# Optimization experiments

Measured on AMD Instinct MI355X. Metric: run time of the kernel, lower is better.

## Reference

```python
import jax, jax.numpy as jnp
import numpy as np

CUTOFF = 5.0

def ssp(x):
    # shifted softplus: ln(0.5*e^x + 0.5)
    return jax.nn.softplus(x) - jnp.log(2.0).astype(x.dtype)

def cosine_cutoff(r):
    return 0.5 * (jnp.cos(jnp.pi * r / CUTOFF) + 1.0) * (r < CUTOFF).astype(r.dtype)

def setup_inputs() -> dict:
    key = jax.random.key(0)
    ks = jax.random.split(key, 16)
    B, A, N, Nd, F, Din, Dout, Th = 2, 512, 1024, 64, 64, 128, 128, 25
    inp = {}
    inp['x'] = jax.random.normal(ks[0], (B, A, Din), dtype=jnp.float32)
    inp['r_double'] = jax.random.uniform(ks[1], (B, A, Nd), dtype=jnp.float32)
    inp['r_ij'] = jax.random.uniform(ks[2], (B, A, N), dtype=jnp.float32)
    inp['r_ik'] = jax.random.uniform(ks[3], (B, A, N), dtype=jnp.float32)
    inp['r_jk'] = jax.random.uniform(ks[4], (B, A, N), dtype=jnp.float32)
    inp['neighbors'] = jax.random.randint(ks[5], (B, A, Nd), 0, A, dtype=jnp.int32)
    inp['neighbor_mask'] = jnp.ones((B, A, Nd), dtype=jnp.float32)
    inp['neighbors_j'] = jax.random.randint(ks[6], (B, A, N), 0, A, dtype=jnp.int32)
    inp['neighbors_k'] = jax.random.randint(ks[7], (B, A, N), 0, A, dtype=jnp.int32)
    inp['triple_masks'] = jnp.ones((B, A, N), dtype=jnp.float32)
    inp['d_ijk'] = jax.random.uniform(ks[8], (B, A, N, Th), dtype=jnp.float32)
    s = 0.1
    inp['W_in2f'] = s * jax.random.normal(ks[9], (Din, F), dtype=jnp.float32)
    inp['W_t1'] = s * jax.random.normal(ks[10], (Th, F), dtype=jnp.float32)
    inp['b_t1'] = jnp.zeros((F,), dtype=jnp.float32)
    inp['W_t2'] = s * jax.random.normal(ks[11], (F, F), dtype=jnp.float32)
    inp['b_t2'] = jnp.zeros((F,), dtype=jnp.float32)
    inp['W_f2out'] = s * jax.random.normal(ks[12], (F, Dout), dtype=jnp.float32)
    inp['b_f2out'] = jnp.zeros((Dout,), dtype=jnp.float32)
    return inp

def reference(x, r_double, r_ij, r_ik, r_jk, neighbors, neighbor_mask,
              neighbors_j, neighbors_k, triple_masks, d_ijk,
              W_in2f, W_t1, b_t1, W_t2, b_t2, W_f2out, b_f2out):
    # Triple filter: 2-layer MLP on angular basis, modulated by cutoffs
    h = ssp(jnp.einsum('bant,tf->banf', d_ijk, W_t1) + b_t1)
    W_triple = jnp.einsum('banf,fg->bang', h, W_t2) + b_t2
    W_triple = W_triple * cosine_cutoff(r_ij)[..., None] * cosine_cutoff(r_ik)[..., None]

    # in2f: (B, A, F)
    y = jnp.einsum('bad,df->baf', x, W_in2f)
    B, A, N = neighbors_j.shape
    F = y.shape[-1]
    # gather neighbor features along atom axis
    yj = jnp.take_along_axis(y, neighbors_j.reshape(B, A * N, 1), axis=1).reshape(B, A, N, F)
    yk = jnp.take_along_axis(y, neighbors_k.reshape(B, A * N, 1), axis=1).reshape(B, A, N, F)
    w_ij = r_ij[..., None]
    w_ik = r_ik[..., None]
    y = (w_ij * yj + w_ik * yk) / (w_ij + w_ik)
    # filter multiply + masked sum aggregation over triples axis
    y = y * W_triple
    y = jnp.sum(y * triple_masks[..., None], axis=2)
    # f2out with shifted-softplus activation
    out = ssp(jnp.einsum('baf,fo->bao', y, W_f2out) + b_f2out)
    return out
```

## Files before the change

kernel.cpp:

```cpp
#include <hip/hip_runtime.h>

#define BB 2
#define AA 512
#define NN 1024
#define FF 64
#define DIN 128
#define DOUT 128
#define TH 25
#define ASTRIDE 40
#define HSTRIDE 72
#define NSPLIT 4
#define BAN_TOTAL (BB * AA * NN)

typedef _Float16 half8 __attribute__((ext_vector_type(8)));
typedef _Float16 half2v __attribute__((ext_vector_type(2)));
typedef float floatx4 __attribute__((ext_vector_type(4)));

__device__ __forceinline__ float ssp_f(float x) {
    return __logf(0.5f * __expf(x) + 0.5f);
}

__device__ __forceinline__ float cutcos(float r) {
    float c = 0.5f * (__cosf(r * (3.14159265358979323846f / 5.0f)) + 1.0f);
    return (r < 5.0f) ? c : 0.0f;
}

#define OFF_Y       0
#define OFF_PARTIAL (OFF_Y + (size_t)BB * AA * FF * 2)
#define OFF_B1      (OFF_PARTIAL + (size_t)NSPLIT * BB * AA * FF * 4)
#define OFF_B2      (OFF_B1 + 4 * 64 * 8 * 2)
#define OFF_BC      (OFF_B2 + 8 * 64 * 8 * 2)
#define OFF_WTAB    (OFF_BC + 4 * 64 * 8)

__global__ void prep_kernel(const float* __restrict__ W_t1, const float* __restrict__ b_t1,
                            const float* __restrict__ W_t2, const float* __restrict__ b_t2,
                            _Float16* __restrict__ B1tab, _Float16* __restrict__ B2tab,
                            float2* __restrict__ bctab) {
    const int lane = threadIdx.x;
    const int quad = lane >> 4;
    const int l16 = lane & 15;
#pragma unroll
    for (int g = 0; g < 4; ++g) {
#pragma unroll
        for (int j = 0; j < 8; ++j) {
            int k = quad * 8 + j;
            B1tab[(g * 64 + lane) * 8 + j] =
                (k < TH) ? (_Float16)W_t1[k * FF + g * 16 + l16] : (_Float16)0.f;
        }
        bctab[g * 64 + lane] = make_float2(b_t1[g * 16 + l16], b_t2[g * 16 + l16]);
#pragma unroll
        for (int q = 0; q < 2; ++q)
#pragma unroll
            for (int j = 0; j < 8; ++j)
                B2tab[((g * 2 + q) * 64 + lane) * 8 + j] =
                    (_Float16)W_t2[(q * 32 + quad * 8 + j) * FF + g * 16 + l16];
    }
}

__global__ void wprep_kernel(const float* __restrict__ r_ij, const float* __restrict__ r_ik,
                             const float* __restrict__ tmask, half2v* __restrict__ wtab) {
    const int i = blockIdx.x * 256 + threadIdx.x;
    float rij = r_ij[i], rik = r_ik[i];
    float inv = cutcos(rij) * cutcos(rik) * tmask[i] / (rij + rik);
    half2v p;
    p[0] = (_Float16)(rij * inv);
    p[1] = (_Float16)(rik * inv);
    wtab[i] = p;
}

__global__ void in2f_kernel(const float* __restrict__ x,
                            const float* __restrict__ Wi,
                            _Float16* __restrict__ y) {
    __shared__ float xs[DIN];
    const int ba = blockIdx.x;
    const int t = threadIdx.x;
    xs[t] = x[ba * DIN + t];
    xs[t + 64] = x[ba * DIN + 64 + t];
    __syncthreads();
    float acc = 0.f;
#pragma unroll 8
    for (int d = 0; d < DIN; ++d) acc += xs[d] * Wi[d * FF + t];
    y[ba * FF + t] = (_Float16)acc;
}

__global__ __launch_bounds__(256) void triple_kernel(
    const int* __restrict__ nbrj, const int* __restrict__ nbrk,
    const float* __restrict__ d_ijk,
    const _Float16* __restrict__ B1tab, const _Float16* __restrict__ B2tab,
    const float2* __restrict__ bctab, const half2v* __restrict__ wtab,
    const _Float16* __restrict__ y_tab, float* __restrict__ partial) {

    __shared__ __align__(16) _Float16 a_tile[4][16 * ASTRIDE];
    __shared__ __align__(16) _Float16 h_tile[4][16 * HSTRIDE];
    __shared__ float red[4][FF];

    const int blk = blockIdx.x;
    const int ba = blk >> 2;
    const int split = blk & 3;
    const int b = ba >> 9;
    const int tid = threadIdx.x;
    const int w = tid >> 6;
    const int lane = tid & 63;
    const int quad = lane >> 4;
    const int l16 = lane & 15;
    const int rA = lane >> 3;
    const int fc = (lane & 7) * 8;

    const long ban = (long)ba * NN;
    const float* dbase = d_ijk + (long)ba * NN * TH;
    const _Float16* yb = y_tab + (long)b * (AA * FF);

    half8 B1[4];
    half8 B2[4][2];
    float b1v[4], b2v[4];
#pragma unroll
    for (int g = 0; g < 4; ++g) {
        B1[g] = *(const half8*)(B1tab + (g * 64 + lane) * 8);
        B2[g][0] = *(const half8*)(B2tab + ((g * 2 + 0) * 64 + lane) * 8);
        B2[g][1] = *(const half8*)(B2tab + ((g * 2 + 1) * 64 + lane) * 8);
        float2 bc = bctab[g * 64 + lane];
        b1v[g] = bc.x;
        b2v[g] = bc.y;
    }

    for (int idx = lane; idx < 16 * 7; idx += 64) {
        int r = idx / 7, c = 25 + idx % 7;
        a_tile[w][r * ASTRIDE + c] = (_Float16)0.f;
    }

    int lofs2[3][2];
#pragma unroll
    for (int m = 0; m < 3; ++m)
#pragma unroll
        for (int e = 0; e < 2; ++e) {
            int s = m * 128 + lane * 2 + e;
            int r = s / TH, c = s - r * TH;
            lofs2[m][e] = r * ASTRIDE + c;
        }
    const int tofs = 15 * ASTRIDE + 9 + lane;

    float acc[8];
#pragma unroll
    for (int i = 0; i < 8; ++i) acc[i] = 0.f;
    const floatx4 zero4 = {0.f, 0.f, 0.f, 0.f};

    float2 pA[3];
    float pT = 0.f;
    half2v pw0, pw1;
    int pj0, pk0, pj1, pk1;
    {
        const int n0 = (split * 16 + w) * 16;
        const float* dsrc = dbase + n0 * TH;
#pragma unroll
        for (int m = 0; m < 3; ++m) pA[m] = *(const float2*)(dsrc + m * 128 + lane * 2);
        if (lane < 16) pT = dsrc[384 + lane];
        const long n0a = ban + n0 + rA;
        const long n1a = n0a + 8;
        pw0 = wtab[n0a];
        pw1 = wtab[n1a];
        pj0 = nbrj[n0a]; pj1 = nbrj[n1a];
        pk0 = nbrk[n0a]; pk1 = nbrk[n1a];
    }

#pragma unroll 1
    for (int it = 0; it < NN / (16 * 4 * NSPLIT); ++it) {
        half8 gj0 = *(const half8*)(yb + pj0 * FF + fc);
        half8 gk0 = *(const half8*)(yb + pk0 * FF + fc);
        half8 gj1 = *(const half8*)(yb + pj1 * FF + fc);
        half8 gk1 = *(const half8*)(yb + pk1 * FF + fc);
        float wj0 = (float)pw0[0], wk0 = (float)pw0[1];
        float wj1 = (float)pw1[0], wk1 = (float)pw1[1];

#pragma unroll
        for (int m = 0; m < 3; ++m) {
            a_tile[w][lofs2[m][0]] = (_Float16)pA[m].x;
            a_tile[w][lofs2[m][1]] = (_Float16)pA[m].y;
        }
        if (lane < 16) a_tile[w][tofs] = (_Float16)pT;

        if (it + 1 < NN / (16 * 4 * NSPLIT)) {
            const int n0 = (split * 16 + (it + 1) * 4 + w) * 16;
            const float* dn = dbase + n0 * TH;
#pragma unroll
            for (int m = 0; m < 3; ++m) pA[m] = *(const float2*)(dn + m * 128 + lane * 2);
            if (lane < 16) pT = dn[384 + lane];
            const long n0a = ban + n0 + rA;
            const long n1a = n0a + 8;
            pw0 = wtab[n0a];
            pw1 = wtab[n1a];
            pj0 = nbrj[n0a]; pj1 = nbrj[n1a];
            pk0 = nbrk[n0a]; pk1 = nbrk[n1a];
        }

        half8 afrag = *(const half8*)&a_tile[w][l16 * ASTRIDE + quad * 8];
#pragma unroll
        for (int g = 0; g < 4; ++g) {
            floatx4 hv = __builtin_amdgcn_mfma_f32_16x16x32_f16(afrag, B1[g], zero4, 0, 0, 0);
#pragma unroll
            for (int r = 0; r < 4; ++r)
                h_tile[w][(quad * 4 + r) * HSTRIDE + g * 16 + l16] =
                    (_Float16)ssp_f(hv[r] + b1v[g]);
        }

        half8 a2q0 = *(const half8*)&h_tile[w][l16 * HSTRIDE + quad * 8];
        half8 a2q1 = *(const half8*)&h_tile[w][l16 * HSTRIDE + 32 + quad * 8];
#pragma unroll
        for (int g = 0; g < 4; ++g) {
            floatx4 w2 = __builtin_amdgcn_mfma_f32_16x16x32_f16(a2q0, B2[g][0], zero4, 0, 0, 0);
            w2 = __builtin_amdgcn_mfma_f32_16x16x32_f16(a2q1, B2[g][1], w2, 0, 0, 0);
#pragma unroll
            for (int r = 0; r < 4; ++r)
                h_tile[w][(quad * 4 + r) * HSTRIDE + g * 16 + l16] =
                    (_Float16)(w2[r] + b2v[g]);
        }
        half8 f0 = *(const half8*)&h_tile[w][rA * HSTRIDE + fc];
        half8 f1 = *(const half8*)&h_tile[w][(8 + rA) * HSTRIDE + fc];

#pragma unroll
        for (int i = 0; i < 8; ++i) {
            float fv0 = wj0 * (float)gj0[i] + wk0 * (float)gk0[i];
            float fv1 = wj1 * (float)gj1[i] + wk1 * (float)gk1[i];
            acc[i] += (float)f0[i] * fv0 + (float)f1[i] * fv1;
        }
    }

#pragma unroll
    for (int i = 0; i < 8; ++i) {
        acc[i] += __shfl_xor(acc[i], 8, 64);
        acc[i] += __shfl_xor(acc[i], 16, 64);
        acc[i] += __shfl_xor(acc[i], 32, 64);
    }
    if (lane < 8)
#pragma unroll
        for (int i = 0; i < 8; ++i) red[w][lane * 8 + i] = acc[i];
    __syncthreads();

    if (tid < FF)
        partial[(split * (BB * AA) + ba) * FF + tid] =
            red[0][tid] + red[1][tid] + red[2][tid] + red[3][tid];
}

__global__ void out_kernel(const float* __restrict__ partial,
                           const float* __restrict__ Wf,
                           const float* __restrict__ bf,
                           float* __restrict__ out) {
    __shared__ float yag[FF];
    const int ba = blockIdx.x;
    const int t = threadIdx.x;
    if (t < FF) {
        float s = 0.f;
#pragma unroll
        for (int sp = 0; sp < NSPLIT; ++sp)
            s += partial[(sp * (BB * AA) + ba) * FF + t];
        yag[t] = s;
    }
    __syncthreads();
    float a = bf[t];
#pragma unroll 8
    for (int f = 0; f < FF; ++f) a += yag[f] * Wf[f * DOUT + t];
    out[(long)ba * DOUT + t] = ssp_f(a);
}

extern "C" void kernel_launch(void* const* d_in, const int* in_sizes, int n_in,
                              void* d_out, int out_size, void* d_ws, size_t ws_size,
                              hipStream_t stream) {
    const float* x       = (const float*)d_in[0];
    const float* r_ij    = (const float*)d_in[2];
    const float* r_ik    = (const float*)d_in[3];
    const int*   nbrj    = (const int*)d_in[7];
    const int*   nbrk    = (const int*)d_in[8];
    const float* tmask   = (const float*)d_in[9];
    const float* d_ijk   = (const float*)d_in[10];
    const float* W_in2f  = (const float*)d_in[11];
    const float* W_t1    = (const float*)d_in[12];
    const float* b_t1    = (const float*)d_in[13];
    const float* W_t2    = (const float*)d_in[14];
    const float* b_t2    = (const float*)d_in[15];
    const float* W_f2out = (const float*)d_in[16];
    const float* b_f2out = (const float*)d_in[17];
    float* out = (float*)d_out;

    char* ws = (char*)d_ws;
    _Float16* y      = (_Float16*)(ws + OFF_Y);
    float* partial   = (float*)(ws + OFF_PARTIAL);
    _Float16* B1tab  = (_Float16*)(ws + OFF_B1);
    _Float16* B2tab  = (_Float16*)(ws + OFF_B2);
    float2* bctab    = (float2*)(ws + OFF_BC);
    half2v* wtab     = (half2v*)(ws + OFF_WTAB);

    prep_kernel<<<1, 64, 0, stream>>>(W_t1, b_t1, W_t2, b_t2, B1tab, B2tab, bctab);
    wprep_kernel<<<BAN_TOTAL / 256, 256, 0, stream>>>(r_ij, r_ik, tmask, wtab);
    in2f_kernel<<<BB * AA, 64, 0, stream>>>(x, W_in2f, y);
    triple_kernel<<<BB * AA * NSPLIT, 256, 0, stream>>>(nbrj, nbrk, d_ijk, B1tab,
                                                        B2tab, bctab, wtab, y, partial);
    out_kernel<<<BB * AA, 128, 0, stream>>>(partial, W_f2out, b_f2out, out);
}
```

Before: 264.6 us.

## Fuse triple-weight prep into triple kernel and use packed half math

Drops the separate wprep kernel. The triple kernel now computes the cutoff-weighted r_ij/r_ik coefficients inline from r_ij, r_ik and the triple mask, which removes the intermediate wtab round-trip. The filter prep kernel is folded into block 0 of the in2f kernel, cutting one launch. The shifted softplus, the bias adds and the neighbour combine/filter multiply switch to packed __half2 arithmetic to lower per-element ALU cost. In exchange, intermediate products are formed in fp16, which reduces accuracy.

Result: no change. 259.6 us (-1.9%).

```diff
diff --git a/kernel.cpp b/kernel.cpp
--- a/kernel.cpp
+++ b/kernel.cpp
@@ -1,4 +1,5 @@
 #include <hip/hip_runtime.h>
+#include <hip/hip_fp16.h>
 
 #define BB 2
 #define AA 512
@@ -10,10 +11,8 @@
 #define ASTRIDE 40
 #define HSTRIDE 72
 #define NSPLIT 4
-#define BAN_TOTAL (BB * AA * NN)
 
 typedef _Float16 half8 __attribute__((ext_vector_type(8)));
-typedef _Float16 half2v __attribute__((ext_vector_type(2)));
 typedef float floatx4 __attribute__((ext_vector_type(4)));
 
 __device__ __forceinline__ float ssp_f(float x) {
@@ -23,6 +22,18 @@
 __device__ __forceinline__ float cutcos(float r) {
     float c = 0.5f * (__cosf(r * (3.14159265358979323846f / 5.0f)) + 1.0f);
     return (r < 5.0f) ? c : 0.0f;
+}
+
+__device__ __forceinline__ __half2 ssp2(__half2 x) {
+    const __half2 hlf = __float2half2_rn(0.5f);
+    return h2log(__hfma2(h2exp(x), hlf, hlf));
+}
+
+__device__ __forceinline__ __half2 pk2(float a, float b) {
+    auto v = __builtin_amdgcn_cvt_pkrtz(a, b);
+    __half2 r;
+    __builtin_memcpy(&r, &v, sizeof(r));
+    return r;
 }
 
 #define OFF_Y       0
@@ -30,47 +41,14 @@
 #define OFF_B1      (OFF_PARTIAL + (size_t)NSPLIT * BB * AA * FF * 4)
 #define OFF_B2      (OFF_B1 + 4 * 64 * 8 * 2)
 #define OFF_BC      (OFF_B2 + 8 * 64 * 8 * 2)
-#define OFF_WTAB    (OFF_BC + 4 * 64 * 8)
-
-__global__ void prep_kernel(const float* __restrict__ W_t1, const float* __restrict__ b_t1,
-                            const float* __restrict__ W_t2, const float* __restrict__ b_t2,
-                            _Float16* __restrict__ B1tab, _Float16* __restrict__ B2tab,
-                            float2* __restrict__ bctab) {
-    const int lane = threadIdx.x;
-    const int quad = lane >> 4;
-    const int l16 = lane & 15;
-#pragma unroll
-    for (int g = 0; g < 4; ++g) {
-#pragma unroll
-        for (int j = 0; j < 8; ++j) {
-            int k = quad * 8 + j;
-            B1tab[(g * 64 + lane) * 8 + j] =
-                (k < TH) ? (_Float16)W_t1[k * FF + g * 16 + l16] : (_Float16)0.f;
-        }
-        bctab[g * 64 + lane] = make_float2(b_t1[g * 16 + l16], b_t2[g * 16 + l16]);
-#pragma unroll
-        for (int q = 0; q < 2; ++q)
-#pragma unroll
-            for (int j = 0; j < 8; ++j)
-                B2tab[((g * 2 + q) * 64 + lane) * 8 + j] =
-                    (_Float16)W_t2[(q * 32 + quad * 8 + j) * FF + g * 16 + l16];
-    }
-}
-
-__global__ void wprep_kernel(const float* __restrict__ r_ij, const float* __restrict__ r_ik,
-                             const float* __restrict__ tmask, half2v* __restrict__ wtab) {
-    const int i = blockIdx.x * 256 + threadIdx.x;
-    float rij = r_ij[i], rik = r_ik[i];
-    float inv = cutcos(rij) * cutcos(rik) * tmask[i] / (rij + rik);
-    half2v p;
-    p[0] = (_Float16)(rij * inv);
-    p[1] = (_Float16)(rik * inv);
-    wtab[i] = p;
-}
-
-__global__ void in2f_kernel(const float* __restrict__ x,
-                            const float* __restrict__ Wi,
-                            _Float16* __restrict__ y) {
+
+__global__ void in2f_prep_kernel(const float* __restrict__ x,
+                                 const float* __restrict__ Wi,
+                                 _Float16* __restrict__ y,
+                                 const float* __restrict__ W_t1, const float* __restrict__ b_t1,
+                                 const float* __restrict__ W_t2, const float* __restrict__ b_t2,
+                                 _Float16* __restrict__ B1tab, _Float16* __restrict__ B2tab,
+                                 float2* __restrict__ bctab) {
     __shared__ float xs[DIN];
     const int ba = blockIdx.x;
     const int t = threadIdx.x;
@@ -81,13 +59,34 @@
 #pragma unroll 8
     for (int d = 0; d < DIN; ++d) acc += xs[d] * Wi[d * FF + t];
     y[ba * FF + t] = (_Float16)acc;
+
+    if (ba == 0) {
+        const int lane = t, quad = t >> 4, l16 = t & 15;
+#pragma unroll
+        for (int g = 0; g < 4; ++g) {
+#pragma unroll
+            for (int j = 0; j < 8; ++j) {
+                int k = quad * 8 + j;
+                B1tab[(g * 64 + lane) * 8 + j] =
+                    (k < TH) ? (_Float16)W_t1[k * FF + g * 16 + l16] : (_Float16)0.f;
+            }
+            bctab[g * 64 + lane] = make_float2(b_t1[g * 16 + l16], b_t2[g * 16 + l16]);
+#pragma unroll
+            for (int q = 0; q < 2; ++q)
+#pragma unroll
+                for (int j = 0; j < 8; ++j)
+                    B2tab[((g * 2 + q) * 64 + lane) * 8 + j] =
+                        (_Float16)W_t2[(q * 32 + quad * 8 + j) * FF + g * 16 + l16];
+        }
+    }
 }
 
 __global__ __launch_bounds__(256) void triple_kernel(
     const int* __restrict__ nbrj, const int* __restrict__ nbrk,
-    const float* __restrict__ d_ijk,
+    const float* __restrict__ r_ij, const float* __restrict__ r_ik,
+    const float* __restrict__ tmask, const float* __restrict__ d_ijk,
     const _Float16* __restrict__ B1tab, const _Float16* __restrict__ B2tab,
-    const float2* __restrict__ bctab, const half2v* __restrict__ wtab,
+    const float2* __restrict__ bctab,
     const _Float16* __restrict__ y_tab, float* __restrict__ partial) {
 
     __shared__ __align__(16) _Float16 a_tile[4][16 * ASTRIDE];
@@ -112,15 +111,15 @@
 
     half8 B1[4];
     half8 B2[4][2];
-    float b1v[4], b2v[4];
+    __half2 b1h[4], b2h[4];
 #pragma unroll
     for (int g = 0; g < 4; ++g) {
         B1[g] = *(const half8*)(B1tab + (g * 64 + lane) * 8);
         B2[g][0] = *(const half8*)(B2tab + ((g * 2 + 0) * 64 + lane) * 8);
         B2[g][1] = *(const half8*)(B2tab + ((g * 2 + 1) * 64 + lane) * 8);
         float2 bc = bctab[g * 64 + lane];
-        b1v[g] = bc.x;
-        b2v[g] = bc.y;
+        b1h[g] = __float2half2_rn(bc.x);
+        b2h[g] = __float2half2_rn(bc.y);
     }
 
     for (int idx = lane; idx < 16 * 7; idx += 64) {
@@ -146,7 +145,7 @@
 
     float2 pA[3];
     float pT = 0.f;
-    half2v pw0, pw1;
+    __half2 pwj0, pwk0, pwj1, pwk1;
     int pj0, pk0, pj1, pk1;
     {
         const int n0 = (split * 16 + w) * 16;
@@ -156,8 +155,12 @@
         if (lane < 16) pT = dsrc[384 + lane];
         const long n0a = ban + n0 + rA;
         const long n1a = n0a + 8;
-        pw0 = wtab[n0a];
-        pw1 = wtab[n1a];
+        float rij0 = r_ij[n0a], rij1 = r_ij[n1a];
+        float rik0 = r_ik[n0a], rik1 = r_ik[n1a];
+        float i0 = cutcos(rij0) * cutcos(rik0) * tmask[n0a] / (rij0 + rik0);
+        float i1 = cutcos(rij1) * cutcos(rik1) * tmask[n1a] / (rij1 + rik1);
+        pwj0 = __float2half2_rn(rij0 * i0); pwk0 = __float2half2_rn(rik0 * i0);
+        pwj1 = __float2half2_rn(rij1 * i1); pwk1 = __float2half2_rn(rik1 * i1);
         pj0 = nbrj[n0a]; pj1 = nbrj[n1a];
         pk0 = nbrk[n0a]; pk1 = nbrk[n1a];
     }
@@ -168,8 +171,7 @@
         half8 gk0 = *(const half8*)(yb + pk0 * FF + fc);
         half8 gj1 = *(const half8*)(yb + pj1 * FF + fc);
         half8 gk1 = *(const half8*)(yb + pk1 * FF + fc);
-        float wj0 = (float)pw0[0], wk0 = (float)pw0[1];
-        float wj1 = (float)pw1[0], wk1 = (float)pw1[1];
+        __half2 wj0 = pwj0, wk0 = pwk0, wj1 = pwj1, wk1 = pwk1;
 
 #pragma unroll
         for (int m = 0; m < 3; ++m) {
@@ -186,8 +188,12 @@
             if (lane < 16) pT = dn[384 + lane];
             const long n0a = ban + n0 + rA;
             const long n1a = n0a + 8;
-            pw0 = wtab[n0a];
-            pw1 = wtab[n1a];
+            float rij0 = r_ij[n0a], rij1 = r_ij[n1a];
+            float rik0 = r_ik[n0a], rik1 = r_ik[n1a];
+            float i0 = cutcos(rij0) * cutcos(rik0) * tmask[n0a] / (rij0 + rik0);
+            float i1 = cutcos(rij1) * cutcos(rik1) * tmask[n1a] / (rij1 + rik1);
+            pwj0 = __float2half2_rn(rij0 * i0); pwk0 = __float2half2_rn(rik0 * i0);
+            pwj1 = __float2half2_rn(rij1 * i1); pwk1 = __float2half2_rn(rik1 * i1);
             pj0 = nbrj[n0a]; pj1 = nbrj[n1a];
             pk0 = nbrk[n0a]; pk1 = nbrk[n1a];
         }
@@ -197,9 +203,14 @@
         for (int g = 0; g < 4; ++g) {
             floatx4 hv = __builtin_amdgcn_mfma_f32_16x16x32_f16(afrag, B1[g], zero4, 0, 0, 0);
 #pragma unroll
-            for (int r = 0; r < 4; ++r)
-                h_tile[w][(quad * 4 + r) * HSTRIDE + g * 16 + l16] =
-                    (_Float16)ssp_f(hv[r] + b1v[g]);
+            for (int p = 0; p < 2; ++p) {
+                __half2 hh = ssp2(__hadd2(pk2(hv[2 * p], hv[2 * p + 1]), b1h[g]));
+                _Float16 lo, hi;
+                __builtin_memcpy(&lo, &hh, 2);
+                __builtin_memcpy(&hi, (char*)&hh + 2, 2);
+                h_tile[w][(quad * 4 + 2 * p) * HSTRIDE + g * 16 + l16] = lo;
+                h_tile[w][(quad * 4 + 2 * p + 1) * HSTRIDE + g * 16 + l16] = hi;
+            }
         }
 
         half8 a2q0 = *(const half8*)&h_tile[w][l16 * HSTRIDE + quad * 8];
@@ -209,18 +220,31 @@
             floatx4 w2 = __builtin_amdgcn_mfma_f32_16x16x32_f16(a2q0, B2[g][0], zero4, 0, 0, 0);
             w2 = __builtin_amdgcn_mfma_f32_16x16x32_f16(a2q1, B2[g][1], w2, 0, 0, 0);
 #pragma unroll
-            for (int r = 0; r < 4; ++r)
-                h_tile[w][(quad * 4 + r) * HSTRIDE + g * 16 + l16] =
-                    (_Float16)(w2[r] + b2v[g]);
+            for (int p = 0; p < 2; ++p) {
+                __half2 fh = __hadd2(pk2(w2[2 * p], w2[2 * p + 1]), b2h[g]);
+                _Float16 lo, hi;
+                __builtin_memcpy(&lo, &fh, 2);
+                __builtin_memcpy(&hi, (char*)&fh + 2, 2);
+                h_tile[w][(quad * 4 + 2 * p) * HSTRIDE + g * 16 + l16] = lo;
+                h_tile[w][(quad * 4 + 2 * p + 1) * HSTRIDE + g * 16 + l16] = hi;
+            }
         }
         half8 f0 = *(const half8*)&h_tile[w][rA * HSTRIDE + fc];
         half8 f1 = *(const half8*)&h_tile[w][(8 + rA) * HSTRIDE + fc];
 
-#pragma unroll
-        for (int i = 0; i < 8; ++i) {
-            float fv0 = wj0 * (float)gj0[i] + wk0 * (float)gk0[i];
-            float fv1 = wj1 * (float)gj1[i] + wk1 * (float)gk1[i];
-            acc[i] += (float)f0[i] * fv0 + (float)f1[i] * fv1;
+        const __half2* gj0p = (const __half2*)&gj0;
+        const __half2* gk0p = (const __half2*)&gk0;
+        const __half2* gj1p = (const __half2*)&gj1;
+        const __half2* gk1p = (const __half2*)&gk1;
+        const __half2* f0p = (const __half2*)&f0;
+        const __half2* f1p = (const __half2*)&f1;
+#pragma unroll
+        for (int p = 0; p < 4; ++p) {
+            __half2 fv0 = __hfma2(wj0, gj0p[p], __hmul2(wk0, gk0p[p]));
+            __half2 fv1 = __hfma2(wj1, gj1p[p], __hmul2(wk1, gk1p[p]));
+            __half2 tot = __hfma2(f1p[p], fv1, __hmul2(f0p[p], fv0));
+            acc[2 * p]     += __low2float(tot);
+            acc[2 * p + 1] += __high2float(tot);
         }
     }
 
@@ -286,12 +310,11 @@
     _Float16* B1tab  = (_Float16*)(ws + OFF_B1);
     _Float16* B2tab  = (_Float16*)(ws + OFF_B2);
     float2* bctab    = (float2*)(ws + OFF_BC);
-    half2v* wtab     = (half2v*)(ws + OFF_WTAB);
-
-    prep_kernel<<<1, 64, 0, stream>>>(W_t1, b_t1, W_t2, b_t2, B1tab, B2tab, bctab);
-    wprep_kernel<<<BAN_TOTAL / 256, 256, 0, stream>>>(r_ij, r_ik, tmask, wtab);
-    in2f_kernel<<<BB * AA, 64, 0, stream>>>(x, W_in2f, y);
-    triple_kernel<<<BB * AA * NSPLIT, 256, 0, stream>>>(nbrj, nbrk, d_ijk, B1tab,
-                                                        B2tab, bctab, wtab, y, partial);
+
+    in2f_prep_kernel<<<BB * AA, 64, 0, stream>>>(x, W_in2f, y, W_t1, b_t1,
+                                                 W_t2, b_t2, B1tab, B2tab, bctab);
+    triple_kernel<<<BB * AA * NSPLIT, 256, 0, stream>>>(nbrj, nbrk, r_ij, r_ik,
+                                                        tmask, d_ijk, B1tab, B2tab,
+                                                        bctab, y, partial);
     out_kernel<<<BB * AA, 128, 0, stream>>>(partial, W_f2out, b_f2out, out);
 }
```
